# Optimization experiments

Measured on AMD Instinct MI355X. Metric: run time of the kernel, lower is better.

Reference implementation:

```python
import jax, jax.numpy as jnp
import numpy as np

DIM = 1024
MEM = 512
HEAD = DIM // 2


def setup_inputs() -> dict:
    key = jax.random.key(0)
    k0, k1, k2, k3, k4 = jax.random.split(key, 5)
    x = jax.random.normal(k0, (4, 8192, DIM), dtype=jnp.float32)
    keys_real = jax.random.normal(k1, (MEM, HEAD), dtype=jnp.float32) * 0.02
    keys_imag = jax.random.normal(k2, (MEM, HEAD), dtype=jnp.float32) * 0.02
    values_real = jax.random.normal(k3, (MEM, HEAD), dtype=jnp.float32) * 0.02
    values_imag = jax.random.normal(k4, (MEM, HEAD), dtype=jnp.float32) * 0.02
    return {"x": x, "keys_real": keys_real, "keys_imag": keys_imag,
            "values_real": values_real, "values_imag": values_imag}


def reference(x, keys_real, keys_imag, values_real, values_imag):
    input_shape = x.shape
    temperature = HEAD ** (-0.5)
    x_flat = x.reshape(-1, DIM)                       # [N, dim]
    q, p = jnp.split(x_flat, 2, axis=-1)              # each [N, head]
    # dual real/imag score matmuls summed -> energy [N, mem]
    energy = jnp.einsum('nh,mh->nm', q, keys_real) + jnp.einsum('nh,mh->nm', p, keys_imag)
    attn = jax.nn.softmax(energy * temperature, axis=-1)
    out_real = jnp.einsum('nm,mh->nh', attn, values_real)
    out_imag = jnp.einsum('nm,mh->nh', attn, values_imag)
    return jnp.concatenate([out_real, out_imag], axis=-1).reshape(input_shape)
```

## Files before the change

kernel.cpp:

```cpp
#include <hip/hip_runtime.h>


#define DIMX   1024
#define MEMN   512
#define NROWS  32768
#define TEMP   0.04419417382415922f

typedef __bf16 bf16;
typedef __bf16 bf16x8 __attribute__((ext_vector_type(8)));
typedef float  f32x4  __attribute__((ext_vector_type(4)));

__device__ __forceinline__ void gload_lds16(const void* g, void* l) {
    __builtin_amdgcn_global_load_lds(
        (const __attribute__((address_space(1))) unsigned*)g,
        (__attribute__((address_space(3))) unsigned*)l,
        16, 0, 0);
}

__global__ __launch_bounds__(256) void pack_kv_kernel(const float* __restrict__ kr,
                                                      const float* __restrict__ ki,
                                                      const float* __restrict__ vr,
                                                      const float* __restrict__ vi,
                                                      bf16* __restrict__ Kb,
                                                      bf16* __restrict__ VbT) {
    const int idx = blockIdx.x * 256 + threadIdx.x;
    {
        const int m = idx >> 10, h = idx & 1023;
        const float v = (h < 512) ? kr[m * 512 + h] : ki[m * 512 + (h - 512)];
        Kb[idx] = (bf16)v;
    }
    {
        const int hp = idx >> 9, m = idx & 511;
        const float v = (hp < 512) ? vr[m * 512 + hp] : vi[m * 512 + (hp - 512)];
        VbT[idx] = (bf16)v;
    }
}

__global__ __launch_bounds__(256, 2) void energy_softmax_kernel(
        const float* __restrict__ x,
        const bf16*  __restrict__ Kb,
        bf16* __restrict__ attn) {
    __shared__ __align__(16) float Xs[64 * 32];
    __shared__ __align__(16) bf16  Ks[512 * 32];
    __shared__ float red[64][4][2];

    const int tid  = threadIdx.x;
    const int wv   = tid >> 6, lane = tid & 63;
    const int lm   = lane & 15, g = lane >> 4;
    const int rowB = blockIdx.x * 64;

    const int xrow = tid >> 3, xchk = tid & 7;
    const int krow = tid >> 2, kchk = tid & 3;

    f32x4 acc[4][8] = {};

    for (int k0 = 0; k0 < DIMX; k0 += 32) {
        __syncthreads();
        #pragma unroll
        for (int li = 0; li < 2; ++li) {
            const int r = li * 32 + xrow;
            gload_lds16(x + (size_t)(rowB + r) * DIMX + k0 + ((xchk ^ (r & 7)) << 2),
                        (char*)Xs + li * 4096 + wv * 1024);
        }
        #pragma unroll
        for (int li = 0; li < 8; ++li) {
            const int r = li * 64 + krow;
            gload_lds16(Kb + (size_t)r * DIMX + k0 + ((kchk ^ ((r >> 1) & 3)) << 3),
                        (char*)Ks + li * 4096 + wv * 1024);
        }
        __syncthreads();

        bf16x8 af[4], bfr[8];
        #pragma unroll
        for (int i = 0; i < 4; ++i) {
            const int r = i * 16 + lm;
            const f32x4 lo = *(const f32x4*)((const char*)Xs + r * 128 + ((( 2*g )    ^ (r & 7)) << 4));
            const f32x4 hi = *(const f32x4*)((const char*)Xs + r * 128 + (((2*g + 1) ^ (r & 7)) << 4));
            bf16x8 a;
            a[0] = (bf16)lo[0]; a[1] = (bf16)lo[1]; a[2] = (bf16)lo[2]; a[3] = (bf16)lo[3];
            a[4] = (bf16)hi[0]; a[5] = (bf16)hi[1]; a[6] = (bf16)hi[2]; a[7] = (bf16)hi[3];
            af[i] = a;
        }
        #pragma unroll
        for (int j = 0; j < 8; ++j) {
            const int r = wv * 128 + j * 16 + lm;
            bfr[j] = *(const bf16x8*)((const char*)Ks + r * 64 + ((g ^ ((r >> 1) & 3)) << 4));
        }

        #pragma unroll
        for (int i = 0; i < 4; ++i)
            #pragma unroll
            for (int j = 0; j < 8; ++j)
                acc[i][j] = __builtin_amdgcn_mfma_f32_16x16x32_bf16(
                    af[i], bfr[j], acc[i][j], 0, 0, 0);
    }

    float fac[4][4];
    #pragma unroll
    for (int i = 0; i < 4; ++i) {
        #pragma unroll
        for (int rg = 0; rg < 4; ++rg) {
            float m = acc[i][0][rg] * TEMP;
            #pragma unroll
            for (int j = 1; j < 8; ++j) m = fmaxf(m, acc[i][j][rg] * TEMP);
            m = fmaxf(m, __shfl_xor(m, 1));
            m = fmaxf(m, __shfl_xor(m, 2));
            m = fmaxf(m, __shfl_xor(m, 4));
            m = fmaxf(m, __shfl_xor(m, 8));
            float s = 0.f;
            #pragma unroll
            for (int j = 0; j < 8; ++j) {
                const float v = __expf(acc[i][j][rg] * TEMP - m);
                acc[i][j][rg] = v;
                s += v;
            }
            s += __shfl_xor(s, 1);
            s += __shfl_xor(s, 2);
            s += __shfl_xor(s, 4);
            s += __shfl_xor(s, 8);
            const int rr = i * 16 + g * 4 + rg;
            if (lm == 0) { red[rr][wv][0] = m; red[rr][wv][1] = s; }
            fac[i][rg] = m;
        }
    }
    __syncthreads();
    #pragma unroll
    for (int i = 0; i < 4; ++i) {
        #pragma unroll
        for (int rg = 0; rg < 4; ++rg) {
            const int rr = i * 16 + g * 4 + rg;
            const float m0 = red[rr][0][0], s0 = red[rr][0][1];
            const float m1 = red[rr][1][0], s1 = red[rr][1][1];
            const float m2 = red[rr][2][0], s2 = red[rr][2][1];
            const float m3 = red[rr][3][0], s3 = red[rr][3][1];
            const float M  = fmaxf(fmaxf(m0, m1), fmaxf(m2, m3));
            const float S  = s0 * __expf(m0 - M) + s1 * __expf(m1 - M)
                           + s2 * __expf(m2 - M) + s3 * __expf(m3 - M);
            fac[i][rg] = __expf(fac[i][rg] - M) / S;
        }
    }
    #pragma unroll
    for (int i = 0; i < 4; ++i) {
        #pragma unroll
        for (int rg = 0; rg < 4; ++rg) {
            const size_t rr = (size_t)(rowB + i * 16 + g * 4 + rg);
            bf16* p = attn + rr * MEMN + wv * 128 + lm;
            const float f = fac[i][rg];
            #pragma unroll
            for (int j = 0; j < 8; ++j)
                p[j * 16] = (bf16)(acc[i][j][rg] * f);
        }
    }
}

template <bool OUT_BF16>
__global__ __launch_bounds__(256) void gemm_bt_kernel(const bf16* __restrict__ A,
                                                      const bf16* __restrict__ Bt,
                                                      void* __restrict__ Cv,
                                                      int M, int N, int K) {
    __shared__ bf16 As[128 * 32];
    __shared__ bf16 Bs[128 * 32];

    const int tid  = threadIdx.x;
    const int wave = tid >> 6, lane = tid & 63;
    const int rowB = blockIdx.y * 128;
    const int colB = blockIdx.x * 128;
    const int wrow = (wave >> 1) * 64;
    const int wcol = (wave & 1) * 64;
    const int lm   = lane & 15;
    const int lkb  = (lane >> 4) * 8;

    const int srow  = tid >> 2;
    const int skcol = (tid & 3) * 8;

    const bf16* Ab = A  + (size_t)rowB * K;
    const bf16* Bb = Bt + (size_t)colB * K;

    f32x4 acc[4][4] = {};

    for (int k0 = 0; k0 < K; k0 += 32) {
        __syncthreads();
        gload_lds16(Ab + (size_t)srow * K + k0 + skcol,        As + wave * 512);
        gload_lds16(Ab + (size_t)(srow + 64) * K + k0 + skcol, As + 2048 + wave * 512);
        gload_lds16(Bb + (size_t)srow * K + k0 + skcol,        Bs + wave * 512);
        gload_lds16(Bb + (size_t)(srow + 64) * K + k0 + skcol, Bs + 2048 + wave * 512);
        __syncthreads();

        bf16x8 af[4], bfr[4];
        #pragma unroll
        for (int i = 0; i < 4; ++i)
            af[i] = *(const bf16x8*)(As + (wrow + i * 16 + lm) * 32 + lkb);
        #pragma unroll
        for (int j = 0; j < 4; ++j)
            bfr[j] = *(const bf16x8*)(Bs + (wcol + j * 16 + lm) * 32 + lkb);

        #pragma unroll
        for (int i = 0; i < 4; ++i)
            #pragma unroll
            for (int j = 0; j < 4; ++j)
                acc[i][j] = __builtin_amdgcn_mfma_f32_16x16x32_bf16(
                    af[i], bfr[j], acc[i][j], 0, 0, 0);
    }

    const int r0 = rowB + wrow + (lane >> 4) * 4;
    const int c0 = colB + wcol + lm;
    #pragma unroll
    for (int i = 0; i < 4; ++i) {
        #pragma unroll
        for (int j = 0; j < 4; ++j) {
            #pragma unroll
            for (int r = 0; r < 4; ++r) {
                const size_t off = (size_t)(r0 + i * 16 + r) * N + (c0 + j * 16);
                if (OUT_BF16) ((bf16*)Cv)[off]  = (bf16)acc[i][j][r];
                else          ((float*)Cv)[off] = acc[i][j][r];
            }
        }
    }
}

extern "C" void kernel_launch(void* const* d_in, const int* in_sizes, int n_in,
                              void* d_out, int out_size, void* d_ws, size_t ws_size,
                              hipStream_t stream) {
    const float* x  = (const float*)d_in[0];
    const float* kr = (const float*)d_in[1];
    const float* ki = (const float*)d_in[2];
    const float* vr = (const float*)d_in[3];
    const float* vi = (const float*)d_in[4];
    float* out = (float*)d_out;

    char* ws = (char*)d_ws;
    bf16* Kb   = (bf16*)ws;
    bf16* VbT  = (bf16*)(ws + 1048576);
    bf16* attn = (bf16*)(ws + 2097152);

    pack_kv_kernel<<<2048, 256, 0, stream>>>(kr, ki, vr, vi, Kb, VbT);
    energy_softmax_kernel<<<512, 256, 0, stream>>>(x, Kb, attn);
    gemm_bt_kernel<false><<<dim3(8, 256), 256, 0, stream>>>(attn, VbT, out,
                                                            NROWS, DIMX, MEMN);
}
```

Before: 332.8 us.

## Double/triple-buffer LDS with register-staged X conversion and swizzled block order

The energy kernel now double-buffers X and K tiles in LDS. X is loaded through registers and converted to bf16 before the LDS write, so the MFMA loop overlaps with the next tile's global loads. The second GEMM gets a triple-buffered prefetch pipeline, uses a flat grid with a remapped block order for L2 locality, and gets an occupancy hint. Manual waitcnt/barrier asm replaces __syncthreads, which cuts sync stalls but adds fragility around vmcnt counts and LDS ordering.

```diff
diff --git a/kernel.cpp b/kernel.cpp
--- a/kernel.cpp
+++ b/kernel.cpp
@@ -16,6 +16,8 @@
         (__attribute__((address_space(3))) unsigned*)l,
         16, 0, 0);
 }
+
+#define WAITBAR(VM) asm volatile("s_waitcnt vmcnt(" #VM ") lgkmcnt(0)\n\ts_barrier" ::: "memory")
 
 __global__ __launch_bounds__(256) void pack_kv_kernel(const float* __restrict__ kr,
                                                       const float* __restrict__ ki,
@@ -40,8 +42,8 @@
         const float* __restrict__ x,
         const bf16*  __restrict__ Kb,
         bf16* __restrict__ attn) {
-    __shared__ __align__(16) float Xs[64 * 32];
-    __shared__ __align__(16) bf16  Ks[512 * 32];
+    __shared__ __align__(16) bf16 Xs[2][64 * 32];
+    __shared__ __align__(16) bf16 Ks[2][512 * 32];
     __shared__ float red[64][4][2];
 
     const int tid  = threadIdx.x;
@@ -49,51 +51,75 @@
     const int lm   = lane & 15, g = lane >> 4;
     const int rowB = blockIdx.x * 64;
 
-    const int xrow = tid >> 3, xchk = tid & 7;
-    const int krow = tid >> 2, kchk = tid & 3;
+    const int sr = tid >> 2;
+    const int sc = tid & 3;
+    const float* xsrc = x + (size_t)(rowB + sr) * DIMX + sc * 8;
+    const int xw_off = sr * 64 + ((sc ^ ((sr >> 1) & 3)) << 4);
 
     f32x4 acc[4][8] = {};
-
-    for (int k0 = 0; k0 < DIMX; k0 += 32) {
-        __syncthreads();
-        #pragma unroll
-        for (int li = 0; li < 2; ++li) {
-            const int r = li * 32 + xrow;
-            gload_lds16(x + (size_t)(rowB + r) * DIMX + k0 + ((xchk ^ (r & 7)) << 2),
-                        (char*)Xs + li * 4096 + wv * 1024);
-        }
-        #pragma unroll
-        for (int li = 0; li < 8; ++li) {
-            const int r = li * 64 + krow;
-            gload_lds16(Kb + (size_t)r * DIMX + k0 + ((kchk ^ ((r >> 1) & 3)) << 3),
-                        (char*)Ks + li * 4096 + wv * 1024);
-        }
-        __syncthreads();
-
-        bf16x8 af[4], bfr[8];
-        #pragma unroll
-        for (int i = 0; i < 4; ++i) {
-            const int r = i * 16 + lm;
-            const f32x4 lo = *(const f32x4*)((const char*)Xs + r * 128 + ((( 2*g )    ^ (r & 7)) << 4));
-            const f32x4 hi = *(const f32x4*)((const char*)Xs + r * 128 + (((2*g + 1) ^ (r & 7)) << 4));
-            bf16x8 a;
-            a[0] = (bf16)lo[0]; a[1] = (bf16)lo[1]; a[2] = (bf16)lo[2]; a[3] = (bf16)lo[3];
-            a[4] = (bf16)hi[0]; a[5] = (bf16)hi[1]; a[6] = (bf16)hi[2]; a[7] = (bf16)hi[3];
-            af[i] = a;
-        }
-        #pragma unroll
-        for (int j = 0; j < 8; ++j) {
-            const int r = wv * 128 + j * 16 + lm;
-            bfr[j] = *(const bf16x8*)((const char*)Ks + r * 64 + ((g ^ ((r >> 1) & 3)) << 4));
-        }
-
-        #pragma unroll
-        for (int i = 0; i < 4; ++i)
-            #pragma unroll
-            for (int j = 0; j < 8; ++j)
-                acc[i][j] = __builtin_amdgcn_mfma_f32_16x16x32_bf16(
-                    af[i], bfr[j], acc[i][j], 0, 0, 0);
-    }
+    f32x4 xa0, xb0, xa1, xb1;
+
+#define K_STAGE(B, K0)                                                          \
+    _Pragma("unroll")                                                           \
+    for (int li = 0; li < 8; ++li) {                                            \
+        const int r = li * 64 + sr;                                             \
+        gload_lds16(Kb + (size_t)r * DIMX + (K0) + ((sc ^ ((r >> 1) & 3)) << 3),\
+                    (char*)Ks[B] + li * 4096 + wv * 1024);                      \
+    }
+
+#define X_ISSUE(A, Bv, K0) { A = *(const f32x4*)(xsrc + (K0));                  \
+                             Bv = *(const f32x4*)(xsrc + (K0) + 4); }
+
+#define X_WRITE(B, A, Bv) { bf16x8 w;                                           \
+    w[0] = (bf16)A[0];  w[1] = (bf16)A[1];  w[2] = (bf16)A[2];  w[3] = (bf16)A[3]; \
+    w[4] = (bf16)Bv[0]; w[5] = (bf16)Bv[1]; w[6] = (bf16)Bv[2]; w[7] = (bf16)Bv[3]; \
+    *(bf16x8*)((char*)Xs[B] + xw_off) = w; }
+
+#define COMPUTE(B) {                                                            \
+    bf16x8 af[4], bfr[8];                                                       \
+    _Pragma("unroll") for (int i = 0; i < 4; ++i) {                             \
+        const int r = i * 16 + lm;                                              \
+        af[i] = *(const bf16x8*)((const char*)Xs[B] + r * 64                    \
+                                 + ((g ^ ((r >> 1) & 3)) << 4));                \
+    }                                                                           \
+    _Pragma("unroll") for (int j = 0; j < 8; ++j) {                             \
+        const int r = wv * 128 + j * 16 + lm;                                   \
+        bfr[j] = *(const bf16x8*)((const char*)Ks[B] + r * 64                   \
+                                  + ((g ^ ((r >> 1) & 3)) << 4));               \
+    }                                                                           \
+    _Pragma("unroll") for (int i = 0; i < 4; ++i)                               \
+        _Pragma("unroll") for (int j = 0; j < 8; ++j)                           \
+            acc[i][j] = __builtin_amdgcn_mfma_f32_16x16x32_bf16(                \
+                af[i], bfr[j], acc[i][j], 0, 0, 0); }
+
+    K_STAGE(0, 0);
+    X_ISSUE(xa0, xb0, 0);
+    X_ISSUE(xa1, xb1, 32);
+    X_WRITE(0, xa0, xb0);
+    WAITBAR(2);
+
+    for (int t = 0; t < 30; t += 2) {
+        K_STAGE(1, (t + 1) * 32);
+        X_ISSUE(xa0, xb0, (t + 2) * 32);
+        COMPUTE(0);
+        X_WRITE(1, xa1, xb1);
+        WAITBAR(2);
+        K_STAGE(0, (t + 2) * 32);
+        X_ISSUE(xa1, xb1, (t + 3) * 32);
+        COMPUTE(1);
+        X_WRITE(0, xa0, xb0);
+        WAITBAR(2);
+    }
+    K_STAGE(1, 31 * 32);
+    COMPUTE(0);
+    X_WRITE(1, xa1, xb1);
+    WAITBAR(0);
+    COMPUTE(1);
+
+#undef K_STAGE
+#undef X_ISSUE
+#undef X_WRITE
+#undef COMPUTE
 
     float fac[4][4];
     #pragma unroll
@@ -154,17 +180,22 @@
 }
 
 template <bool OUT_BF16>
-__global__ __launch_bounds__(256) void gemm_bt_kernel(const bf16* __restrict__ A,
-                                                      const bf16* __restrict__ Bt,
-                                                      void* __restrict__ Cv,
-                                                      int M, int N, int K) {
-    __shared__ bf16 As[128 * 32];
-    __shared__ bf16 Bs[128 * 32];
+__global__ __launch_bounds__(256, 2) void gemm_bt_kernel(const bf16* __restrict__ A,
+                                                         const bf16* __restrict__ Bt,
+                                                         void* __restrict__ Cv,
+                                                         int M, int N, int K) {
+    __shared__ bf16 As[3][128 * 32];
+    __shared__ bf16 Bs[3][128 * 32];
+
+    const int cpx = gridDim.x >> 3;
+    const int l   = (blockIdx.x & 7) * cpx + (blockIdx.x >> 3);
+    const int nbx = N >> 7;
+    const int bx  = l & (nbx - 1), by = l / nbx;
 
     const int tid  = threadIdx.x;
     const int wave = tid >> 6, lane = tid & 63;
-    const int rowB = blockIdx.y * 128;
-    const int colB = blockIdx.x * 128;
+    const int rowB = by * 128;
+    const int colB = bx * 128;
     const int wrow = (wave >> 1) * 64;
     const int wcol = (wave & 1) * 64;
     const int lm   = lane & 15;
@@ -178,29 +209,38 @@
 
     f32x4 acc[4][4] = {};
 
-    for (int k0 = 0; k0 < K; k0 += 32) {
-        __syncthreads();
-        gload_lds16(Ab + (size_t)srow * K + k0 + skcol,        As + wave * 512);
-        gload_lds16(Ab + (size_t)(srow + 64) * K + k0 + skcol, As + 2048 + wave * 512);
-        gload_lds16(Bb + (size_t)srow * K + k0 + skcol,        Bs + wave * 512);
-        gload_lds16(Bb + (size_t)(srow + 64) * K + k0 + skcol, Bs + 2048 + wave * 512);
-        __syncthreads();
-
-        bf16x8 af[4], bfr[4];
-        #pragma unroll
-        for (int i = 0; i < 4; ++i)
-            af[i] = *(const bf16x8*)(As + (wrow + i * 16 + lm) * 32 + lkb);
-        #pragma unroll
-        for (int j = 0; j < 4; ++j)
-            bfr[j] = *(const bf16x8*)(Bs + (wcol + j * 16 + lm) * 32 + lkb);
-
-        #pragma unroll
-        for (int i = 0; i < 4; ++i)
-            #pragma unroll
-            for (int j = 0; j < 4; ++j)
-                acc[i][j] = __builtin_amdgcn_mfma_f32_16x16x32_bf16(
-                    af[i], bfr[j], acc[i][j], 0, 0, 0);
-    }
+#define STAGE(B, K0) {                                                          \
+    gload_lds16(Ab + (size_t)srow * K + (K0) + skcol,        As[B] + wave * 512); \
+    gload_lds16(Ab + (size_t)(srow + 64) * K + (K0) + skcol, As[B] + 2048 + wave * 512); \
+    gload_lds16(Bb + (size_t)srow * K + (K0) + skcol,        Bs[B] + wave * 512); \
+    gload_lds16(Bb + (size_t)(srow + 64) * K + (K0) + skcol, Bs[B] + 2048 + wave * 512); }
+
+#define G2_COMPUTE(B) {                                                         \
+    bf16x8 af[4], bfr[4];                                                       \
+    _Pragma("unroll") for (int i = 0; i < 4; ++i)                               \
+        af[i] = *(const bf16x8*)(As[B] + (wrow + i * 16 + lm) * 32 + lkb);      \
+    _Pragma("unroll") for (int j = 0; j < 4; ++j)                               \
+        bfr[j] = *(const bf16x8*)(Bs[B] + (wcol + j * 16 + lm) * 32 + lkb);     \
+    _Pragma("unroll") for (int i = 0; i < 4; ++i)                               \
+        _Pragma("unroll") for (int j = 0; j < 4; ++j)                           \
+            acc[i][j] = __builtin_amdgcn_mfma_f32_16x16x32_bf16(                \
+                af[i], bfr[j], acc[i][j], 0, 0, 0); }
+
+    STAGE(0, 0);
+    STAGE(1, 32);
+    WAITBAR(4);
+    for (int t = 0; t < 12; t += 3) {
+        STAGE(2, (t + 2) * 32); G2_COMPUTE(0); WAITBAR(4);
+        STAGE(0, (t + 3) * 32); G2_COMPUTE(1); WAITBAR(4);
+        STAGE(1, (t + 4) * 32); G2_COMPUTE(2); WAITBAR(4);
+    }
+    STAGE(2, 14 * 32); G2_COMPUTE(0); WAITBAR(4);
+    STAGE(0, 15 * 32); G2_COMPUTE(1); WAITBAR(4);
+    G2_COMPUTE(2);                   WAITBAR(0);
+    G2_COMPUTE(0);
+
+#undef STAGE
+#undef G2_COMPUTE
 
     const int r0 = rowB + wrow + (lane >> 4) * 4;
     const int c0 = colB + wcol + lm;
@@ -235,6 +275,6 @@
 
     pack_kv_kernel<<<2048, 256, 0, stream>>>(kr, ki, vr, vi, Kb, VbT);
     energy_softmax_kernel<<<512, 256, 0, stream>>>(x, Kb, attn);
-    gemm_bt_kernel<false><<<dim3(8, 256), 256, 0, stream>>>(attn, VbT, out,
-                                                            NROWS, DIMX, MEMN);
-}
+    gemm_bt_kernel<false><<<2048, 256, 0, stream>>>(attn, VbT, out,
+                                                    NROWS, DIMX, MEMN);
+}
```

After: 317.8 us. -4.5%, faster.

## Pre-swizzle K/V into MFMA fragment order and double-buffer both GEMMs

Applied to the files above, without the earlier changes.

The pack kernel now writes K and V in MFMA-fragment tile order, so each lane can load B operands straight from global memory into registers and skip LDS. The energy kernel converts x to bf16 once while writing it to a double-buffered LDS tile, and prefetches the next K chunk into registers during MFMA work, using explicit waitcnt/barrier asm. The second GEMM gets a similar double-buffered A staging with register-prefetched V, a 1D grid with block-index swizzling for L2 locality, and launch bounds raised to three blocks per CU. The aim is to hide global latency and cut LDS traffic and the duplicated bf16 conversion. The cost is fragile hand-written vmcnt counting and higher register pressure.

```diff
diff --git a/kernel.cpp b/kernel.cpp
--- a/kernel.cpp
+++ b/kernel.cpp
@@ -16,23 +16,38 @@
         (__attribute__((address_space(3))) unsigned*)l,
         16, 0, 0);
 }
+__device__ __forceinline__ void gl_b16x8(bf16x8& d, const bf16* p) {
+    asm volatile("global_load_dwordx4 %0, %1, off" : "=v"(d) : "v"(p));
+}
+__device__ __forceinline__ void gl_f32x4(f32x4& d, const float* p) {
+    asm volatile("global_load_dwordx4 %0, %1, off" : "=v"(d) : "v"(p));
+}
+#define VMW(N)     do { asm volatile("s_waitcnt vmcnt(" #N ")" ::: "memory"); \
+                        __builtin_amdgcn_sched_barrier(0); } while (0)
+#define WAITBAR(N) do { asm volatile("s_waitcnt vmcnt(" #N ") lgkmcnt(0)\n\t" \
+                        "s_barrier" ::: "memory");                            \
+                        __builtin_amdgcn_sched_barrier(0); } while (0)
 
 __global__ __launch_bounds__(256) void pack_kv_kernel(const float* __restrict__ kr,
                                                       const float* __restrict__ ki,
                                                       const float* __restrict__ vr,
                                                       const float* __restrict__ vi,
                                                       bf16* __restrict__ Kb,
-                                                      bf16* __restrict__ VbT) {
+                                                      bf16* __restrict__ Vb) {
     const int idx = blockIdx.x * 256 + threadIdx.x;
+    const int e = idx & 7, l = (idx >> 3) & 63;
+    const int lm = l & 15, g = l >> 4;
     {
-        const int m = idx >> 10, h = idx & 1023;
-        const float v = (h < 512) ? kr[m * 512 + h] : ki[m * 512 + (h - 512)];
+        const int t = (idx >> 9) & 31, c = idx >> 14;
+        const int row = t * 16 + lm, k = c * 32 + g * 8 + e;
+        const float v = (k < 512) ? kr[row * 512 + k] : ki[row * 512 + (k - 512)];
         Kb[idx] = (bf16)v;
     }
     {
-        const int hp = idx >> 9, m = idx & 511;
-        const float v = (hp < 512) ? vr[m * 512 + hp] : vi[m * 512 + (hp - 512)];
-        VbT[idx] = (bf16)v;
+        const int t = (idx >> 9) & 63, c = idx >> 15;
+        const int h = t * 16 + lm, m = c * 32 + g * 8 + e;
+        const float v = (h < 512) ? vr[m * 512 + h] : vi[m * 512 + (h - 512)];
+        Vb[idx] = (bf16)v;
     }
 }
 
@@ -40,8 +55,7 @@
         const float* __restrict__ x,
         const bf16*  __restrict__ Kb,
         bf16* __restrict__ attn) {
-    __shared__ __align__(16) float Xs[64 * 32];
-    __shared__ __align__(16) bf16  Ks[512 * 32];
+    __shared__ __align__(16) bf16 Xs[2][64 * 32];
     __shared__ float red[64][4][2];
 
     const int tid  = threadIdx.x;
@@ -49,51 +63,61 @@
     const int lm   = lane & 15, g = lane >> 4;
     const int rowB = blockIdx.x * 64;
 
-    const int xrow = tid >> 3, xchk = tid & 7;
-    const int krow = tid >> 2, kchk = tid & 3;
+    const int sr = tid >> 2, sc = tid & 3;
+    const float* xsrc = x + (size_t)(rowB + sr) * DIMX + sc * 8;
+    const int xw_off = sr * 64 + ((sc ^ ((sr >> 1) & 3)) << 4);
+
+    const bf16* kbase = Kb + (wv * 8) * 512 + lane * 8;
 
     f32x4 acc[4][8] = {};
-
-    for (int k0 = 0; k0 < DIMX; k0 += 32) {
-        __syncthreads();
-        #pragma unroll
-        for (int li = 0; li < 2; ++li) {
-            const int r = li * 32 + xrow;
-            gload_lds16(x + (size_t)(rowB + r) * DIMX + k0 + ((xchk ^ (r & 7)) << 2),
-                        (char*)Xs + li * 4096 + wv * 1024);
-        }
-        #pragma unroll
-        for (int li = 0; li < 8; ++li) {
-            const int r = li * 64 + krow;
-            gload_lds16(Kb + (size_t)r * DIMX + k0 + ((kchk ^ ((r >> 1) & 3)) << 3),
-                        (char*)Ks + li * 4096 + wv * 1024);
-        }
-        __syncthreads();
-
-        bf16x8 af[4], bfr[8];
-        #pragma unroll
-        for (int i = 0; i < 4; ++i) {
-            const int r = i * 16 + lm;
-            const f32x4 lo = *(const f32x4*)((const char*)Xs + r * 128 + ((( 2*g )    ^ (r & 7)) << 4));
-            const f32x4 hi = *(const f32x4*)((const char*)Xs + r * 128 + (((2*g + 1) ^ (r & 7)) << 4));
-            bf16x8 a;
-            a[0] = (bf16)lo[0]; a[1] = (bf16)lo[1]; a[2] = (bf16)lo[2]; a[3] = (bf16)lo[3];
-            a[4] = (bf16)hi[0]; a[5] = (bf16)hi[1]; a[6] = (bf16)hi[2]; a[7] = (bf16)hi[3];
-            af[i] = a;
-        }
-        #pragma unroll
-        for (int j = 0; j < 8; ++j) {
-            const int r = wv * 128 + j * 16 + lm;
-            bfr[j] = *(const bf16x8*)((const char*)Ks + r * 64 + ((g ^ ((r >> 1) & 3)) << 4));
-        }
-
-        #pragma unroll
-        for (int i = 0; i < 4; ++i)
-            #pragma unroll
-            for (int j = 0; j < 8; ++j)
-                acc[i][j] = __builtin_amdgcn_mfma_f32_16x16x32_bf16(
-                    af[i], bfr[j], acc[i][j], 0, 0, 0);
-    }
+    f32x4 xa, xb;
+    bf16x8 bA[8], bB[8];
+
+#define K_PREF(DST, C) { _Pragma("unroll") for (int j = 0; j < 8; ++j)         \
+        gl_b16x8(DST[j], kbase + (size_t)(C) * 16384 + j * 512); }
+#define X_PREF(S) { gl_f32x4(xa, xsrc + (S) * 32);                             \
+                    gl_f32x4(xb, xsrc + (S) * 32 + 4); }
+#define X_WR(B) { bf16x8 w;                                                    \
+    w[0]=(bf16)xa[0]; w[1]=(bf16)xa[1]; w[2]=(bf16)xa[2]; w[3]=(bf16)xa[3];    \
+    w[4]=(bf16)xb[0]; w[5]=(bf16)xb[1]; w[6]=(bf16)xb[2]; w[7]=(bf16)xb[3];    \
+    *(bf16x8*)((char*)Xs[B] + xw_off) = w; }
+#define COMPUTE_E(XB, BF) { bf16x8 af[4];                                      \
+    _Pragma("unroll") for (int i = 0; i < 4; ++i) { const int r = i * 16 + lm; \
+        af[i] = *(const bf16x8*)((const char*)Xs[XB] + r * 64                  \
+                                 + ((g ^ ((r >> 1) & 3)) << 4)); }             \
+    _Pragma("unroll") for (int i = 0; i < 4; ++i)                              \
+        _Pragma("unroll") for (int j = 0; j < 8; ++j)                          \
+            acc[i][j] = __builtin_amdgcn_mfma_f32_16x16x32_bf16(               \
+                af[i], BF[j], acc[i][j], 0, 0, 0); }
+
+    X_PREF(0);
+    K_PREF(bA, 0);
+    VMW(8);  X_WR(0);
+    X_PREF(1);
+    WAITBAR(2);
+
+    for (int t = 0; t < 30; t += 2) {
+        K_PREF(bB, t + 1);
+        COMPUTE_E(0, bA);
+        VMW(8);  X_WR(1);
+        X_PREF(t + 2);
+        WAITBAR(2);
+        K_PREF(bA, t + 2);
+        COMPUTE_E(1, bB);
+        VMW(8);  X_WR(0);
+        X_PREF(t + 3);
+        WAITBAR(2);
+    }
+    K_PREF(bB, 31);
+    COMPUTE_E(0, bA);
+    VMW(8);  X_WR(1);
+    WAITBAR(0);
+    COMPUTE_E(1, bB);
+
+#undef K_PREF
+#undef X_PREF
+#undef X_WR
+#undef COMPUTE_E
 
     float fac[4][4];
     #pragma unroll
@@ -153,67 +177,68 @@
     }
 }
 
-template <bool OUT_BF16>
-__global__ __launch_bounds__(256) void gemm_bt_kernel(const bf16* __restrict__ A,
-                                                      const bf16* __restrict__ Bt,
-                                                      void* __restrict__ Cv,
-                                                      int M, int N, int K) {
-    __shared__ bf16 As[128 * 32];
-    __shared__ bf16 Bs[128 * 32];
+__global__ __launch_bounds__(256, 3) void gemm2_kernel(const bf16* __restrict__ A,
+                                                       const bf16* __restrict__ Vb,
+                                                       float* __restrict__ C) {
+    __shared__ __align__(16) bf16 As[2][128 * 32];
+
+    const int cpx = gridDim.x >> 3;
+    const int l   = ((int)blockIdx.x & 7) * cpx + ((int)blockIdx.x >> 3);
+    const int bx  = l & 7, by = l >> 3;
 
     const int tid  = threadIdx.x;
     const int wave = tid >> 6, lane = tid & 63;
-    const int rowB = blockIdx.y * 128;
-    const int colB = blockIdx.x * 128;
+    const int lm   = lane & 15, g = lane >> 4;
+    const int rowB = by * 128;
     const int wrow = (wave >> 1) * 64;
-    const int wcol = (wave & 1) * 64;
-    const int lm   = lane & 15;
-    const int lkb  = (lane >> 4) * 8;
-
-    const int srow  = tid >> 2;
-    const int skcol = (tid & 3) * 8;
-
-    const bf16* Ab = A  + (size_t)rowB * K;
-    const bf16* Bb = Bt + (size_t)colB * K;
+
+    const bf16* vbase = Vb + (bx * 8 + (wave & 1) * 4) * 512 + lane * 8;
 
     f32x4 acc[4][4] = {};
-
-    for (int k0 = 0; k0 < K; k0 += 32) {
-        __syncthreads();
-        gload_lds16(Ab + (size_t)srow * K + k0 + skcol,        As + wave * 512);
-        gload_lds16(Ab + (size_t)(srow + 64) * K + k0 + skcol, As + 2048 + wave * 512);
-        gload_lds16(Bb + (size_t)srow * K + k0 + skcol,        Bs + wave * 512);
-        gload_lds16(Bb + (size_t)(srow + 64) * K + k0 + skcol, Bs + 2048 + wave * 512);
-        __syncthreads();
-
-        bf16x8 af[4], bfr[4];
-        #pragma unroll
-        for (int i = 0; i < 4; ++i)
-            af[i] = *(const bf16x8*)(As + (wrow + i * 16 + lm) * 32 + lkb);
-        #pragma unroll
-        for (int j = 0; j < 4; ++j)
-            bfr[j] = *(const bf16x8*)(Bs + (wcol + j * 16 + lm) * 32 + lkb);
-
-        #pragma unroll
-        for (int i = 0; i < 4; ++i)
-            #pragma unroll
-            for (int j = 0; j < 4; ++j)
-                acc[i][j] = __builtin_amdgcn_mfma_f32_16x16x32_bf16(
-                    af[i], bfr[j], acc[i][j], 0, 0, 0);
-    }
-
-    const int r0 = rowB + wrow + (lane >> 4) * 4;
-    const int c0 = colB + wcol + lm;
+    bf16x8 bA[4], bB[4];
+
+#define STAGE_A(B, C0) { _Pragma("unroll") for (int li = 0; li < 2; ++li) {     \
+        const int q = wave * 2 + li;                                            \
+        const int r = q * 16 + (lane >> 2);                                     \
+        const int ch = lane & 3;                                                \
+        gload_lds16(A + (size_t)(rowB + r) * 512 + (C0) * 32                    \
+                      + ((ch ^ ((r >> 1) & 3)) << 3),                           \
+                    (char*)As[B] + q * 1024); } }
+#define B_PREF(DST, C0) { _Pragma("unroll") for (int j = 0; j < 4; ++j)         \
+        gl_b16x8(DST[j], vbase + (size_t)(C0) * 32768 + j * 512); }
+#define COMPUTE_G(XB, BF) { bf16x8 af[4];                                       \
+    _Pragma("unroll") for (int i = 0; i < 4; ++i) {                             \
+        const int r = wrow + i * 16 + lm;                                       \
+        af[i] = *(const bf16x8*)((const char*)As[XB] + r * 64                   \
+                                 + ((g ^ ((r >> 1) & 3)) << 4)); }              \
+    _Pragma("unroll") for (int i = 0; i < 4; ++i)                               \
+        _Pragma("unroll") for (int j = 0; j < 4; ++j)                           \
+            acc[i][j] = __builtin_amdgcn_mfma_f32_16x16x32_bf16(                \
+                af[i], BF[j], acc[i][j], 0, 0, 0); }
+
+    STAGE_A(0, 0);
+    B_PREF(bA, 0);
+    WAITBAR(0);
+    for (int t = 0; t < 14; t += 2) {
+        STAGE_A(1, t + 1); B_PREF(bB, t + 1); COMPUTE_G(0, bA); WAITBAR(0);
+        STAGE_A(0, t + 2); B_PREF(bA, t + 2); COMPUTE_G(1, bB); WAITBAR(0);
+    }
+    STAGE_A(1, 15); B_PREF(bB, 15); COMPUTE_G(0, bA); WAITBAR(0);
+    COMPUTE_G(1, bB);
+
+#undef STAGE_A
+#undef B_PREF
+#undef COMPUTE_G
+
+    const int r0 = rowB + wrow + g * 4;
+    const int c0 = bx * 128 + (wave & 1) * 64 + lm;
     #pragma unroll
     for (int i = 0; i < 4; ++i) {
         #pragma unroll
         for (int j = 0; j < 4; ++j) {
             #pragma unroll
-            for (int r = 0; r < 4; ++r) {
-                const size_t off = (size_t)(r0 + i * 16 + r) * N + (c0 + j * 16);
-                if (OUT_BF16) ((bf16*)Cv)[off]  = (bf16)acc[i][j][r];
-                else          ((float*)Cv)[off] = acc[i][j][r];
-            }
+            for (int r = 0; r < 4; ++r)
+                C[(size_t)(r0 + i * 16 + r) * DIMX + (c0 + j * 16)] = acc[i][j][r];
         }
     }
 }
@@ -230,11 +255,10 @@
 
     char* ws = (char*)d_ws;
     bf16* Kb   = (bf16*)ws;
-    bf16* VbT  = (bf16*)(ws + 1048576);
+    bf16* Vb   = (bf16*)(ws + 1048576);
     bf16* attn = (bf16*)(ws + 2097152);
 
-    pack_kv_kernel<<<2048, 256, 0, stream>>>(kr, ki, vr, vi, Kb, VbT);
+    pack_kv_kernel<<<2048, 256, 0, stream>>>(kr, ki, vr, vi, Kb, Vb);
     energy_softmax_kernel<<<512, 256, 0, stream>>>(x, Kb, attn);
-    gemm_bt_kernel<false><<<dim3(8, 256), 256, 0, stream>>>(attn, VbT, out,
-                                                            NROWS, DIMX, MEMN);
-}
+    gemm2_kernel<<<2048, 256, 0, stream>>>(attn, Vb, out);
+}
```

New measurement: 292.8 us. 12.0% less time.
